# Performance work log

Measured on AMD Instinct MI355X. Metric: run time of the kernel, lower is better.

## Reference

```python
import jax, jax.numpy as jnp
import numpy as np

D, H, N, BS = 3072, 2048, 16, 512
MAX_LATENT_VAR = 0.1


def setup_inputs() -> dict:
    key = jax.random.key(0)
    ks = jax.random.split(key, 12)
    s = 0.02
    return {
        "x": jax.random.normal(ks[0], (BS, D), dtype=jnp.float32),
        "eps": jax.random.normal(ks[1], (1, BS, N), dtype=jnp.float32),
        "enc_W1": jax.random.normal(ks[2], (D, H), dtype=jnp.float32) * s,
        "enc_b1": jnp.zeros((H,), dtype=jnp.float32),
        "enc_Wmu": jax.random.normal(ks[3], (H, N), dtype=jnp.float32) * s,
        "enc_bmu": jnp.zeros((N,), dtype=jnp.float32),
        "enc_Wls": jax.random.normal(ks[4], (H, 1), dtype=jnp.float32) * s,
        "enc_bls": jnp.zeros((1,), dtype=jnp.float32),
        "dec_W1": jax.random.normal(ks[5], (N, H), dtype=jnp.float32) * 0.1,
        "dec_b1": jnp.zeros((H,), dtype=jnp.float32),
        "dec_W2": jax.random.normal(ks[6], (H, D), dtype=jnp.float32) * s,
        "dec_b2": jnp.zeros((D,), dtype=jnp.float32),
    }


def reference(x, eps, enc_W1, enc_b1, enc_Wmu, enc_bmu, enc_Wls, enc_bls,
              dec_W1, dec_b1, dec_W2, dec_b2):
    bs, Dd = x.shape
    n = dec_W1.shape[0]

    def dec(z):  # smooth 2-layer MLP decoder (supports nested autodiff)
        return jnp.tanh(z @ dec_W1 + dec_b1) @ dec_W2 + dec_b2

    # encoder.forward_with_sigma
    h = jnp.tanh(x @ enc_W1 + enc_b1)
    z_star = h @ enc_Wmu + enc_bmu                      # (bs, n)
    sigma = jnp.exp(h @ enc_Wls + enc_bls)[:, 0]        # (bs,)

    # per-sample Jacobian of decoder: (bs, D, n)
    J = jax.vmap(jax.jacfwd(dec))(z_star)

    # per-sample Hessian of f(z) = stop_grad(d) . d,  d = (x - dec(z)) / sigma
    def f_hess(z, xi, sg):
        d = (xi - dec(z)) / sg
        return jnp.dot(jax.lax.stop_gradient(d), d)
    hess = jax.vmap(jax.hessian(f_hess), in_axes=(0, 0, 0))(z_star, x, sigma)  # (bs,n,n)

    eye = jnp.eye(n, dtype=x.dtype)
    Prec = jnp.einsum('bdi,bdj->bij', J, J) / (sigma ** 2)[:, None, None] + eye + hess

    eigvals = jnp.linalg.eigvalsh(Prec)                 # ascending, (bs, n)
    eigmin = eigvals[:, 0]
    delta = 1.0 / MAX_LATENT_VAR - eigmin               # (bs,)
    Prec = Prec + eye * delta[:, None, None]
    eigvals = eigvals + delta[:, None]

    # upper-triangular Cholesky: U^T U = Prec
    U = jnp.swapaxes(jnp.linalg.cholesky(Prec), -1, -2)  # (bs, n, n)

    def solve1(u, e):  # solve U y = e
        return jax.scipy.linalg.solve_triangular(u, e[:, None], lower=False)[:, 0]
    z_off = jax.vmap(jax.vmap(solve1, in_axes=(0, 0)), in_axes=(None, 0))(U, eps)  # (ne,bs,n)
    z_sample = z_star[None] + z_off

    n_eval = eps.shape[0]
    recon = dec(z_sample.reshape(-1, n)).reshape(n_eval, bs, Dd)
    recon_loss = ((recon - x[None]) ** 2).sum(axis=2).mean(axis=0) / (2.0 * sigma ** 2)
    latent_energy = (z_star ** 2).sum(axis=1) / 2.0 + (1.0 / eigvals).sum(axis=1) / 2.0
    logdet_loss = jnp.log(eigvals).sum(axis=1) / 2.0
    sigma_loss = Dd * jnp.log(sigma)
    neg_log_prob = (recon_loss + latent_energy + logdet_loss + sigma_loss) / Dd
    return (neg_log_prob, recon_loss, latent_energy, logdet_loss, sigma)
```

## Files before the change

### kernel.cpp

```cpp
#include <hip/hip_runtime.h>
#include <hip/hip_bf16.h>
#include <math.h>

#define D_ 3072
#define H_ 2048
#define N_ 16
#define BS_ 512

typedef short s16x8 __attribute__((ext_vector_type(8)));
typedef float f32x4v __attribute__((ext_vector_type(4)));
typedef __hip_bfloat16 bf16;

__device__ __forceinline__ void gload_lds16(const void* g, void* l) {
    __builtin_amdgcn_global_load_lds((const __attribute__((address_space(1))) void*)g,
                                     (__attribute__((address_space(3))) void*)l, 16, 0, 0);
}

__device__ __forceinline__ float bf2f(unsigned short u) {
    unsigned v = (unsigned)u << 16; float f; __builtin_memcpy(&f, &v, 4); return f;
}

__global__ __launch_bounds__(256) void mfma_nt_sk(
    const bf16* __restrict__ A, const bf16* __restrict__ Bt,
    float* __restrict__ C, int M, int N, int K, int KC)
{
    __shared__ __align__(16) bf16 As[128 * 32];
    __shared__ __align__(16) bf16 Bs[128 * 32];
    const int tid = threadIdx.x;
    const int w = tid >> 6, l = tid & 63;
    const int wr = w >> 1, wc = w & 1;
    const int m0 = blockIdx.y * 128, n0 = blockIdx.x * 128;
    const int kbeg = blockIdx.z * KC;

    f32x4v acc[4][4];
    #pragma unroll
    for (int a = 0; a < 4; ++a)
        #pragma unroll
        for (int b = 0; b < 4; ++b) acc[a][b] = (f32x4v){0.f, 0.f, 0.f, 0.f};

    const int srow = l >> 2;
    const int scol = (l & 3) * 8;

    for (int k0 = kbeg; k0 < kbeg + KC; k0 += 32) {
        #pragma unroll
        for (int q = 0; q < 2; ++q) {
            int r0 = w * 32 + q * 16;
            gload_lds16(&A[(size_t)(m0 + r0 + srow) * K + k0 + scol], &As[r0 * 32]);
            gload_lds16(&Bt[(size_t)(n0 + r0 + srow) * K + k0 + scol], &Bs[r0 * 32]);
        }
        __syncthreads();
        s16x8 af[4], bfr[4];
        #pragma unroll
        for (int mf = 0; mf < 4; ++mf)
            af[mf] = *(const s16x8*)&As[(wr * 64 + mf * 16 + (l & 15)) * 32 + (l >> 4) * 8];
        #pragma unroll
        for (int nf = 0; nf < 4; ++nf)
            bfr[nf] = *(const s16x8*)&Bs[(wc * 64 + nf * 16 + (l & 15)) * 32 + (l >> 4) * 8];
        #pragma unroll
        for (int mf = 0; mf < 4; ++mf)
            #pragma unroll
            for (int nf = 0; nf < 4; ++nf)
                acc[mf][nf] = __builtin_amdgcn_mfma_f32_16x16x32_bf16(af[mf], bfr[nf], acc[mf][nf], 0, 0, 0);
        __syncthreads();
    }

    #pragma unroll
    for (int mf = 0; mf < 4; ++mf)
        #pragma unroll
        for (int nf = 0; nf < 4; ++nf) {
            int n = n0 + wc * 64 + nf * 16 + (l & 15);
            #pragma unroll
            for (int r = 0; r < 4; ++r) {
                int m = m0 + wr * 64 + mf * 16 + (l >> 4) * 4 + r;
                atomicAdd(&C[(size_t)m * N + n], acc[mf][nf][r]);
            }
        }
}

__global__ __launch_bounds__(256) void ep_ebf(const float* __restrict__ C,
    const float* __restrict__ bias, const float* __restrict__ X,
    bf16* __restrict__ Eout, int MN, int N)
{
    int base = (blockIdx.x * 256 + threadIdx.x) * 8;
    if (base < MN) {
        float4 c0 = *(const float4*)&C[base];
        float4 c1 = *(const float4*)&C[base + 4];
        float4 x0 = *(const float4*)&X[base];
        float4 x1 = *(const float4*)&X[base + 4];
        int n = base % N;
        float4 b0 = *(const float4*)&bias[n];
        float4 b1 = *(const float4*)&bias[n + 4];
        union { s16x8 v; bf16 e[8]; } u;
        u.e[0] = __float2bfloat16(x0.x - (c0.x + b0.x));
        u.e[1] = __float2bfloat16(x0.y - (c0.y + b0.y));
        u.e[2] = __float2bfloat16(x0.z - (c0.z + b0.z));
        u.e[3] = __float2bfloat16(x0.w - (c0.w + b0.w));
        u.e[4] = __float2bfloat16(x1.x - (c1.x + b1.x));
        u.e[5] = __float2bfloat16(x1.y - (c1.y + b1.y));
        u.e[6] = __float2bfloat16(x1.z - (c1.z + b1.z));
        u.e[7] = __float2bfloat16(x1.w - (c1.w + b1.w));
        *(s16x8*)&Eout[base] = u.v;
    }
}

__global__ __launch_bounds__(256) void ep_recon(const float* __restrict__ C,
    const float* __restrict__ bias, const float* __restrict__ X, float* __restrict__ rls)
{
    int m = blockIdx.x;
    float s = 0.f;
    for (int n = threadIdx.x * 4; n < D_; n += 1024) {
        float4 c = *(const float4*)&C[(size_t)m * D_ + n];
        float4 bb = *(const float4*)&bias[n];
        float4 xx = *(const float4*)&X[(size_t)m * D_ + n];
        float v0 = c.x + bb.x - xx.x, v1 = c.y + bb.y - xx.y;
        float v2 = c.z + bb.z - xx.z, v3 = c.w + bb.w - xx.w;
        s += v0 * v0 + v1 * v1 + v2 * v2 + v3 * v3;
    }
    __shared__ float red[4];
    int wid = threadIdx.x >> 6, lane = threadIdx.x & 63;
    #pragma unroll
    for (int off = 32; off; off >>= 1) s += __shfl_xor(s, off);
    if (lane == 0) red[wid] = s;
    __syncthreads();
    if (threadIdx.x == 0) rls[m] = red[0] + red[1] + red[2] + red[3];
}

__global__ __launch_bounds__(256) void jtj_fused(
    const bf16* __restrict__ Vt, const bf16* __restrict__ W2t,
    float* __restrict__ S, int Mb, int b0)
{
    __shared__ union {
        struct { __align__(16) bf16 As[3][128 * 32]; __align__(16) bf16 Bs[3][128 * 32]; } s;
        __align__(16) bf16 J[128 * 136];
    } u;
    const int tid = threadIdx.x;
    const int w = tid >> 6, l = tid & 63;
    const int wr = w >> 1, wc = w & 1;

    int mb, nbk;
    if ((Mb & 7) == 0) {
        int lin = blockIdx.y * 24 + blockIdx.x;
        int xcd = lin & 7, idx = lin >> 3;
        int mchunk = Mb >> 3;
        mb = xcd * mchunk + idx / 24;
        nbk = idx % 24;
    } else { mb = blockIdx.y; nbk = blockIdx.x; }
    const int m0 = mb * 128, n0 = nbk * 128;

    f32x4v acc[4][4];
    #pragma unroll
    for (int a = 0; a < 4; ++a)
        #pragma unroll
        for (int b = 0; b < 4; ++b) acc[a][b] = (f32x4v){0.f, 0.f, 0.f, 0.f};

    const int strow = tid >> 2;
    const int scb = (((tid & 3) ^ ((tid >> 3) & 3)) << 4);

    auto STAGE = [&](int kt, int bi) {
        const char* a0 = (const char*)Vt  + ((size_t)(m0 + strow) * H_ + kt * 32) * 2 + scb;
        const char* b0p = (const char*)W2t + ((size_t)(n0 + strow) * H_ + kt * 32) * 2 + scb;
        char* la = (char*)u.s.As[bi] + w * 1024;
        char* lb = (char*)u.s.Bs[bi] + w * 1024;
        gload_lds16(a0, la);
        gload_lds16(a0 + (size_t)64 * H_ * 2, la + 4096);
        gload_lds16(b0p, lb);
        gload_lds16(b0p + (size_t)64 * H_ * 2, lb + 4096);
    };

    STAGE(0, 0);
    STAGE(1, 1);

    const int rdcb = (((l >> 4) ^ ((l >> 1) & 3)) << 4);

    for (int kt = 0; kt < H_ / 32; ++kt) {
        __builtin_amdgcn_sched_barrier(0);
        if (kt == H_ / 32 - 1) asm volatile("s_waitcnt vmcnt(0)" ::: "memory");
        else                   asm volatile("s_waitcnt vmcnt(4)" ::: "memory");
        __builtin_amdgcn_s_barrier();
        __builtin_amdgcn_sched_barrier(0);
        const int cur = kt % 3;
        const char* Ab = (const char*)u.s.As[cur];
        const char* Bb = (const char*)u.s.Bs[cur];
        s16x8 af[4], bfr[4];
        #pragma unroll
        for (int mf = 0; mf < 4; ++mf)
            af[mf] = *(const s16x8*)(Ab + (wr * 64 + mf * 16 + (l & 15)) * 64 + rdcb);
        #pragma unroll
        for (int nf = 0; nf < 4; ++nf)
            bfr[nf] = *(const s16x8*)(Bb + (wc * 64 + nf * 16 + (l & 15)) * 64 + rdcb);
        if (kt + 2 < H_ / 32) STAGE(kt + 2, (kt + 2) % 3);
        #pragma unroll
        for (int mf = 0; mf < 4; ++mf)
            #pragma unroll
            for (int nf = 0; nf < 4; ++nf)
                acc[mf][nf] = __builtin_amdgcn_mfma_f32_16x16x32_bf16(af[mf], bfr[nf], acc[mf][nf], 0, 0, 0);
    }

    __syncthreads();
    #pragma unroll
    for (int mf = 0; mf < 4; ++mf) {
        int rbase = wr * 64 + mf * 16 + (l >> 4) * 4;
        #pragma unroll
        for (int nf = 0; nf < 4; ++nf) {
            int col = wc * 64 + nf * 16 + (l & 15);
            #pragma unroll
            for (int r = 0; r < 4; ++r)
                u.J[(rbase + r) * 136 + col] = __float2bfloat16(acc[mf][nf][r]);
        }
    }
    __syncthreads();

    #pragma unroll
    for (int t2 = 0; t2 < 2; ++t2) {
        int bl = w * 2 + t2;
        f32x4v sp = (f32x4v){0.f, 0.f, 0.f, 0.f};
        #pragma unroll
        for (int kq = 0; kq < 4; ++kq) {
            s16x8 fr = *(const s16x8*)&u.J[(bl * 16 + (l & 15)) * 136 + kq * 32 + (l >> 4) * 8];
            sp = __builtin_amdgcn_mfma_f32_16x16x32_bf16(fr, fr, sp, 0, 0, 0);
        }
        int bglob = b0 + mb * 8 + bl;
        #pragma unroll
        for (int r = 0; r < 4; ++r)
            atomicAdd(&S[(size_t)bglob * 256 + ((l >> 4) * 4 + r) * 16 + (l & 15)], sp[r]);
    }
}

__global__ __launch_bounds__(256) void hess_mfma(const float* __restrict__ t,
    const float* __restrict__ g, const bf16* __restrict__ W1b, float* __restrict__ S)
{
    const int w = threadIdx.x >> 6, l = threadIdx.x & 63;
    const int b = blockIdx.x * 4 + w;
    const int row = l & 15, kq = (l >> 4) * 8;

    f32x4v sp = (f32x4v){0.f, 0.f, 0.f, 0.f};
    for (int k0 = 0; k0 < H_; k0 += 32) {
        int kk = k0 + kq;
        s16x8 wf = *(const s16x8*)&W1b[(size_t)row * H_ + kk];
        float4 t0 = *(const float4*)&t[(size_t)b * H_ + kk];
        float4 t1 = *(const float4*)&t[(size_t)b * H_ + kk + 4];
        float4 g0 = *(const float4*)&g[(size_t)b * H_ + kk];
        float4 g1 = *(const float4*)&g[(size_t)b * H_ + kk + 4];
        float wv[8];
        wv[0] = 2.f * g0.x * t0.x * (1.f - t0.x * t0.x);
        wv[1] = 2.f * g0.y * t0.y * (1.f - t0.y * t0.y);
        wv[2] = 2.f * g0.z * t0.z * (1.f - t0.z * t0.z);
        wv[3] = 2.f * g0.w * t0.w * (1.f - t0.w * t0.w);
        wv[4] = 2.f * g1.x * t1.x * (1.f - t1.x * t1.x);
        wv[5] = 2.f * g1.y * t1.y * (1.f - t1.y * t1.y);
        wv[6] = 2.f * g1.z * t1.z * (1.f - t1.z * t1.z);
        wv[7] = 2.f * g1.w * t1.w * (1.f - t1.w * t1.w);
        union { s16x8 v; bf16 e[8]; } af;
        #pragma unroll
        for (int e = 0; e < 8; ++e)
            af.e[e] = __float2bfloat16(wv[e] * bf2f((unsigned short)wf[e]));
        sp = __builtin_amdgcn_mfma_f32_16x16x32_bf16(af.v, wf, sp, 0, 0, 0);
    }
    #pragma unroll
    for (int r = 0; r < 4; ++r)
        S[(size_t)b * 256 + ((l >> 4) * 4 + r) * 16 + (l & 15)] += sp[r];
}

__global__ __launch_bounds__(256) void prep_all(
    const float* __restrict__ x, const float* __restrict__ enc_W1,
    const float* __restrict__ dec_W2, const float* __restrict__ dec_W1,
    bf16* __restrict__ x_bf, bf16* __restrict__ eW1t,
    bf16* __restrict__ W2t, bf16* __restrict__ W2b, bf16* __restrict__ W1b)
{
    __shared__ float tile[64][65];
    const int blk = blockIdx.x;
    const int tid = threadIdx.x;
    if (blk < 768) {
        int i = blk * 256 + tid;
        const float4* p = (const float4*)x + (size_t)i * 2;
        float4 a = p[0], b = p[1];
        union { s16x8 v; bf16 e[8]; } u;
        u.e[0] = __float2bfloat16(a.x); u.e[1] = __float2bfloat16(a.y);
        u.e[2] = __float2bfloat16(a.z); u.e[3] = __float2bfloat16(a.w);
        u.e[4] = __float2bfloat16(b.x); u.e[5] = __float2bfloat16(b.y);
        u.e[6] = __float2bfloat16(b.z); u.e[7] = __float2bfloat16(b.w);
        *(s16x8*)&x_bf[(size_t)i * 8] = u.v;
    } else if (blk < 768 + 1536) {
        int bid = blk - 768;
        int r0 = (bid % 48) * 64, c0 = (bid / 48) * 64;
        int tx = tid & 63, ty = tid >> 6;
        #pragma unroll
        for (int k = 0; k < 16; ++k) {
            int rr = ty * 16 + k;
            tile[rr][tx] = enc_W1[(size_t)(r0 + rr) * H_ + c0 + tx];
        }
        __syncthreads();
        #pragma unroll
        for (int k = 0; k < 16; ++k) {
            int cc = ty * 16 + k;
            eW1t[(size_t)(c0 + cc) * D_ + r0 + tx] = __float2bfloat16(tile[tx][cc]);
        }
    } else if (blk < 768 + 3072) {
        int bid = blk - 768 - 1536;
        int r0 = (bid % 32) * 64, c0 = (bid / 32) * 64;
        int tx = tid & 63, ty = tid >> 6;
        #pragma unroll
        for (int k = 0; k < 16; ++k) {
            int rr = ty * 16 + k;
            float v = dec_W2[(size_t)(r0 + rr) * D_ + c0 + tx];
            tile[rr][tx] = v;
            W2b[(size_t)(r0 + rr) * D_ + c0 + tx] = __float2bfloat16(v);
        }
        __syncthreads();
        #pragma unroll
        for (int k = 0; k < 16; ++k) {
            int cc = ty * 16 + k;
            W2t[(size_t)(c0 + cc) * H_ + r0 + tx] = __float2bfloat16(tile[tx][cc]);
        }
    } else {
        int i = (blk - 768 - 3072) * 256 + tid;
        if (i < N_ * H_ / 8) {
            const float4* p = (const float4*)dec_W1 + (size_t)i * 2;
            float4 a = p[0], b = p[1];
            union { s16x8 v; bf16 e[8]; } u;
            u.e[0] = __float2bfloat16(a.x); u.e[1] = __float2bfloat16(a.y);
            u.e[2] = __float2bfloat16(a.z); u.e[3] = __float2bfloat16(a.w);
            u.e[4] = __float2bfloat16(b.x); u.e[5] = __float2bfloat16(b.y);
            u.e[6] = __float2bfloat16(b.z); u.e[7] = __float2bfloat16(b.w);
            *(s16x8*)&W1b[(size_t)i * 8] = u.v;
        }
    }
}

__global__ __launch_bounds__(256) void zsig_t_kernel(const float* __restrict__ Ch,
    const float* __restrict__ enc_b1, const float* __restrict__ Wmu, const float* __restrict__ bmu,
    const float* __restrict__ Wls, const float* __restrict__ bls,
    const float* __restrict__ dW1, const float* __restrict__ db1,
    float* __restrict__ z_star, float* __restrict__ lsig, float* __restrict__ sigma,
    float* __restrict__ t, bf16* __restrict__ tb)
{
    const int b = blockIdx.x, tid = threadIdx.x;
    float acc[17];
    #pragma unroll
    for (int i = 0; i < 17; ++i) acc[i] = 0.f;
    for (int hh = tid; hh < H_; hh += 256) {
        float hv = tanhf(Ch[(size_t)b * H_ + hh] + enc_b1[hh]);
        const float* wr = &Wmu[(size_t)hh * 16];
        #pragma unroll
        for (int i = 0; i < 16; ++i) acc[i] += hv * wr[i];
        acc[16] += hv * Wls[hh];
    }
    __shared__ float red[17][4];
    __shared__ float zs[16];
    const int wid = tid >> 6, lane = tid & 63;
    #pragma unroll
    for (int i = 0; i < 17; ++i) {
        float v = acc[i];
        #pragma unroll
        for (int off = 32; off; off >>= 1) v += __shfl_xor(v, off);
        if (lane == 0) red[i][wid] = v;
    }
    __syncthreads();
    if (tid < 17) {
        float v = red[tid][0] + red[tid][1] + red[tid][2] + red[tid][3];
        if (tid < 16) { float z = v + bmu[tid]; zs[tid] = z; z_star[(size_t)b * 16 + tid] = z; }
        else { float ls = v + bls[0]; lsig[b] = ls; sigma[b] = expf(ls); }
    }
    __syncthreads();
    for (int hh = tid; hh < H_; hh += 256) {
        float a = db1[hh];
        #pragma unroll
        for (int i = 0; i < 16; ++i) a += zs[i] * dW1[(size_t)i * H_ + hh];
        float tv = tanhf(a);
        t[(size_t)b * H_ + hh] = tv;
        tb[(size_t)b * H_ + hh] = __float2bfloat16(tv);
    }
}

__global__ __launch_bounds__(256) void build_t(const float* __restrict__ z,
    const float* __restrict__ W1, const float* __restrict__ b1, bf16* __restrict__ tb)
{
    __shared__ float zs[16];
    int b = blockIdx.x, tid = threadIdx.x;
    if (tid < 16) zs[tid] = z[(size_t)b * 16 + tid];
    __syncthreads();
    for (int hh = tid; hh < H_; hh += 256) {
        float a = b1[hh];
        #pragma unroll
        for (int i = 0; i < 16; ++i) a += zs[i] * W1[(size_t)i * H_ + hh];
        tb[(size_t)b * H_ + hh] = __float2bfloat16(tanhf(a));
    }
}

__global__ __launch_bounds__(256) void build_vt(const float* __restrict__ t,
    const float* __restrict__ W1, bf16* __restrict__ Vt, int b0)
{
    int bl = blockIdx.x, b = b0 + bl, tid = threadIdx.x;
    __shared__ float u[H_];
    for (int hh = tid; hh < H_; hh += 256) {
        float tv = t[(size_t)b * H_ + hh];
        u[hh] = 1.f - tv * tv;
    }
    __syncthreads();
    size_t base = (size_t)bl * 16 * H_;
    int hh = tid * 8;
    for (int i = 0; i < 16; ++i) {
        union { s16x8 v; bf16 e[8]; } pk;
        #pragma unroll
        for (int k = 0; k < 8; ++k)
            pk.e[k] = __float2bfloat16(u[hh + k] * W1[(size_t)i * H_ + hh + k]);
        *(s16x8*)&Vt[base + (size_t)i * H_ + hh] = pk.v;
    }
}

__global__ __launch_bounds__(64) void solve_kernel(const float* __restrict__ S,
    const float* __restrict__ sigma, const float* __restrict__ z_star,
    const float* __restrict__ eps, float* __restrict__ z_sample, float* __restrict__ d_out)
{
    const int lane = threadIdx.x;
    const int q = lane >> 4;
    const int j = lane & 15;
    const int b = blockIdx.x * 4 + q;

    const float sg = sigma[b];
    const float inv_s2 = 1.0f / (sg * sg);

    float a0[16], a[16];
    #pragma unroll
    for (int r = 0; r < 16; ++r) {
        a0[r] = S[(size_t)b * 256 + r * 16 + j] * inv_s2 + ((r == j) ? 1.0f : 0.0f);
        a[r] = a0[r];
    }

    #pragma unroll
    for (int k = 0; k < 14; ++k) {
        float x[16];
        #pragma unroll
        for (int r = 0; r < 16; ++r) x[r] = __shfl(a[k], r, 16);
        float sig2 = 0.f;
        #pragma unroll
        for (int r = 0; r < 16; ++r) if (r > k + 1) sig2 += x[r] * x[r];
        float x0 = x[k + 1];
        float normx = sqrtf(sig2 + x0 * x0);
        float alpha = (x0 >= 0.f) ? -normx : normx;
        float v[16];
        #pragma unroll
        for (int r = 0; r < 16; ++r)
            v[r] = (r <= k) ? 0.f : ((r == k + 1) ? x0 - alpha : x[r]);
        float vtv = 0.f;
        #pragma unroll
        for (int r = 0; r < 16; ++r) vtv += v[r] * v[r];
        float beta = (vtv > 1e-28f) ? 2.0f / vtv : 0.f;
        float sj = 0.f;
        #pragma unroll
        for (int r = 0; r < 16; ++r) sj += a[r] * v[r];
        float av[16];
        #pragma unroll
        for (int r = 0; r < 16; ++r) av[r] = __shfl(sj, r, 16);
        float vtav = 0.f;
        #pragma unroll
        for (int r = 0; r < 16; ++r) vtav += v[r] * av[r];
        float c = 0.5f * beta * vtav;
        float wv[16];
        #pragma unroll
        for (int r = 0; r < 16; ++r) wv[r] = beta * (av[r] - c * v[r]);
        float vj = (j <= k) ? 0.f : ((j == k + 1) ? a[k] - alpha : a[k]);
        float wj = beta * (sj - c * vj);
        #pragma unroll
        for (int r = 0; r < 16; ++r) a[r] -= v[r] * wj + wv[r] * vj;
    }

    float dg[16], eo[15];
    #pragma unroll
    for (int r = 0; r < 16; ++r) dg[r] = __shfl(a[r], r, 16);
    #pragma unroll
    for (int r = 0; r < 15; ++r) eo[r] = __shfl(a[r + 1], r, 16);

    float lo = 1e30f, hi = 1e30f;
    #pragma unroll
    for (int r = 0; r < 16; ++r) {
        float rad = ((r > 0) ? fabsf(eo[r - 1]) : 0.f) + ((r < 15) ? fabsf(eo[r]) : 0.f);
        lo = fminf(lo, dg[r] - rad);
        hi = fminf(hi, dg[r]);
    }
    lo -= 1e-4f; hi += 1e-4f;

    #pragma unroll
    for (int pass = 0; pass < 5; ++pass) {
        float step = (hi - lo) * (1.0f / 17.0f);
        float s = lo + step * (float)(j + 1);
        float qq = dg[0] - s;
        int cnt = (qq < 0.f) ? 1 : 0;
        #pragma unroll
        for (int i = 1; i < 16; ++i) {
            float denom = (fabsf(qq) < 1e-30f) ? -1e-30f : qq;
            qq = dg[i] - s - eo[i - 1] * eo[i - 1] / denom;
            cnt += (qq < 0.f) ? 1 : 0;
        }
        unsigned long long bal = __ballot(cnt >= 1);
        unsigned grp = (unsigned)((bal >> (q * 16)) & 0xffffull);
        int f = grp ? (__ffs(grp) - 1) : 16;
        float nlo = lo + step * (float)f;
        float nhi = (f < 16) ? (lo + step * (float)(f + 1)) : hi;
        lo = nlo; hi = nhi;
    }
    const float lam_min = 0.5f * (lo + hi);
    const float delta = 10.0f - lam_min;

    float bm[16];
    #pragma unroll
    for (int r = 0; r < 16; ++r) bm[r] = a0[r] + ((r == j) ? delta : 0.f);

    float ldsum = 0.f;
    #pragma unroll
    for (int kk = 0; kk < 16; ++kk) {
        float ck[16];
        #pragma unroll
        for (int r = 0; r < 16; ++r) ck[r] = __shfl(bm[kk], r, 16);
        float dkk = sqrtf(fmaxf(ck[kk], 1e-30f));
        float inv = 1.0f / dkk;
        ldsum += logf(dkk);
        float lfull[16];
        #pragma unroll
        for (int r = 0; r < 16; ++r) lfull[r] = ck[r] * inv;
        float lj = bm[kk] * inv;
        if (j == kk) {
            #pragma unroll
            for (int r = 0; r < 16; ++r) bm[r] = (r >= kk) ? lfull[r] : 0.f;
        } else if (j > kk) {
            #pragma unroll
            for (int r = 0; r < 16; ++r)
                if (r > kk) bm[r] -= lfull[r] * lj;
        }
    }

    float w[16];
    #pragma unroll
    for (int r = 0; r < 16; ++r) w[r] = 0.f;
    #pragma unroll
    for (int i = 0; i < 16; ++i) {
        float row[16];
        #pragma unroll
        for (int kx = 0; kx < 16; ++kx) row[kx] = __shfl(bm[i], kx, 16);
        float sacc = 0.f;
        #pragma unroll
        for (int kx = 0; kx < 16; ++kx) if (kx < i) sacc += row[kx] * w[kx];
        float invd = 1.0f / row[i];
        float val = (i == j) ? invd : (-sacc * invd);
        w[i] = (i >= j) ? val : 0.f;
    }

    float tsum = 0.f;
    #pragma unroll
    for (int r = 0; r < 16; ++r) tsum += w[r] * w[r];
    float zv = z_star[(size_t)b * 16 + j];
    float ep = eps[(size_t)b * 16 + j];
    float epsv[16];
    #pragma unroll
    for (int r = 0; r < 16; ++r) epsv[r] = __shfl(ep, r, 16);
    float zoff = 0.f;
    #pragma unroll
    for (int r = 0; r < 16; ++r) zoff += w[r] * epsv[r];
    z_sample[(size_t)b * 16 + j] = zv + zoff;

    float zsq = zv * zv;
    #pragma unroll
    for (int off = 1; off < 16; off <<= 1) {
        tsum += __shfl_xor(tsum, off);
        zsq  += __shfl_xor(zsq, off);
    }
    if (j == 0) {
        d_out[2 * 512 + b] = 0.5f * zsq + 0.5f * tsum;
        d_out[3 * 512 + b] = ldsum;
        d_out[4 * 512 + b] = sg;
    }
}

__global__ void finalize_kernel(const float* __restrict__ rlsum, const float* __restrict__ sigma,
    const float* __restrict__ lsig, float* __restrict__ d_out)
{
    int b = blockIdx.x * 256 + threadIdx.x;
    if (b < BS_) {
        float sg = sigma[b];
        float rl = rlsum[b] / (2.0f * sg * sg);
        float le = d_out[2 * 512 + b];
        float ld = d_out[3 * 512 + b];
        d_out[b] = (rl + le + ld) / 3072.0f + lsig[b];
        d_out[512 + b] = rl;
    }
}

extern "C" void kernel_launch(void* const* d_in, const int* in_sizes, int n_in,
                              void* d_out, int out_size, void* d_ws, size_t ws_size,
                              hipStream_t stream)
{
    const float* x       = (const float*)d_in[0];
    const float* eps     = (const float*)d_in[1];
    const float* enc_W1  = (const float*)d_in[2];
    const float* enc_b1  = (const float*)d_in[3];
    const float* enc_Wmu = (const float*)d_in[4];
    const float* enc_bmu = (const float*)d_in[5];
    const float* enc_Wls = (const float*)d_in[6];
    const float* enc_bls = (const float*)d_in[7];
    const float* dec_W1  = (const float*)d_in[8];
    const float* dec_b1  = (const float*)d_in[9];
    const float* dec_W2  = (const float*)d_in[10];
    const float* dec_b2  = (const float*)d_in[11];
    float* out = (float*)d_out;

    char* wsb = (char*)d_ws;
    size_t off = 0;
    auto alloc = [&](size_t bytes) -> void* {
        off = (off + 255) & ~(size_t)255;
        void* p = wsb + off;
        off += bytes;
        return p;
    };

    float* Ch   = (float*)alloc((size_t)BS_ * H_ * 4);
    float* Cd   = (float*)alloc((size_t)BS_ * D_ * 4);
    float* g    = (float*)alloc((size_t)BS_ * H_ * 4);
    float* S    = (float*)alloc((size_t)BS_ * 256 * 4);
    size_t zero_span = (size_t)((char*)(S + BS_ * 256) - (char*)Ch);

    float* t    = (float*)alloc((size_t)BS_ * H_ * 4);
    float* z_st = (float*)alloc((size_t)BS_ * 16 * 4);
    float* lsig = (float*)alloc(BS_ * 4);
    float* sigm = (float*)alloc(BS_ * 4);
    float* z_sm = (float*)alloc((size_t)BS_ * 16 * 4);
    float* rls  = (float*)alloc(BS_ * 4);
    bf16* x_bf  = (bf16*)alloc((size_t)BS_ * D_ * 2);
    bf16* eW1t  = (bf16*)alloc((size_t)H_ * D_ * 2);
    bf16* W2b   = (bf16*)alloc((size_t)H_ * D_ * 2);
    bf16* W2t   = (bf16*)alloc((size_t)D_ * H_ * 2);
    bf16* W1b   = (bf16*)alloc((size_t)N_ * H_ * 2);
    bf16* t_bf  = (bf16*)alloc((size_t)BS_ * H_ * 2);
    bf16* e_bf  = (bf16*)alloc((size_t)BS_ * D_ * 2);
    bf16* t2b   = (bf16*)alloc((size_t)BS_ * H_ * 2);

    int nb = 0;
    size_t base_off = off;
    const int cand[3] = {512, 128, 32};
    bf16* Vt = nullptr;
    for (int ci = 0; ci < 3; ++ci) {
        off = base_off;
        int n = cand[ci];
        bf16* vt = (bf16*)alloc((size_t)n * 16 * H_ * 2);
        if (off <= ws_size) { nb = n; Vt = vt; break; }
    }
    if (nb == 0) return;

    prep_all<<<dim3(768 + 3072 + 16), 256, 0, stream>>>(
        x, enc_W1, dec_W2, dec_W1, x_bf, eW1t, W2t, W2b, W1b);
    hipMemsetAsync(Ch, 0, zero_span, stream);

    mfma_nt_sk<<<dim3(H_ / 128, BS_ / 128, 4), 256, 0, stream>>>(
        x_bf, eW1t, Ch, BS_, H_, D_, D_ / 4);
    zsig_t_kernel<<<dim3(BS_), 256, 0, stream>>>(Ch, enc_b1, enc_Wmu, enc_bmu, enc_Wls, enc_bls,
        dec_W1, dec_b1, z_st, lsig, sigm, t, t_bf);
    mfma_nt_sk<<<dim3(D_ / 128, BS_ / 128, 4), 256, 0, stream>>>(
        t_bf, W2t, Cd, BS_, D_, H_, H_ / 4);
    ep_ebf<<<dim3(BS_ * D_ / 8 / 256), 256, 0, stream>>>(Cd, dec_b2, x, e_bf, BS_ * D_, D_);
    mfma_nt_sk<<<dim3(H_ / 128, BS_ / 128, 4), 256, 0, stream>>>(
        e_bf, W2b, g, BS_, H_, D_, D_ / 4);

    for (int b0 = 0; b0 < BS_; b0 += nb) {
        build_vt<<<dim3(nb), 256, 0, stream>>>(t, dec_W1, Vt, b0);
        jtj_fused<<<dim3(D_ / 128, nb * 16 / 128), 256, 0, stream>>>(
            Vt, W2t, S, nb * 16 / 128, b0);
    }
    hess_mfma<<<dim3(BS_ / 4), 256, 0, stream>>>(t, g, W1b, S);

    solve_kernel<<<dim3(BS_ / 4), 64, 0, stream>>>(S, sigm, z_st, eps, z_sm, out);
    build_t<<<dim3(BS_), 256, 0, stream>>>(z_sm, dec_W1, dec_b1, t2b);
    hipMemsetAsync(Cd, 0, (size_t)BS_ * D_ * 4, stream);
    mfma_nt_sk<<<dim3(D_ / 128, BS_ / 128, 4), 256, 0, stream>>>(
        t2b, W2t, Cd, BS_, D_, H_, H_ / 4);
    ep_recon<<<dim3(BS_), 256, 0, stream>>>(Cd, dec_b2, x, rls);
    finalize_kernel<<<dim3(2), 256, 0, stream>>>(rls, sigm, lsig, out);
}
```

Before: 359.5 us.

## Replace split-K atomics with per-slice slabs and fuse Vt build and finalize

Three of the four split-K GEMMs now write each K slice to its own fp32 slab with plain stores instead of atomicAdd, and the consumer kernels (zsig_t, ep_ebf, ep_recon) sum the four slabs. This removes the atomic traffic and the large memsets of the Ch and Cd buffers. The Vt construction is fused into zsig_t_kernel when the whole batch fits, which drops the separate build_vt launches, and finalize is folded into ep_recon. In exchange it uses four times the scratch memory for these outputs, and consumers must read four times as much data.

```diff
diff --git a/kernel.cpp b/kernel.cpp
--- a/kernel.cpp
+++ b/kernel.cpp
@@ -20,7 +20,7 @@
     unsigned v = (unsigned)u << 16; float f; __builtin_memcpy(&f, &v, 4); return f;
 }
 
-__global__ __launch_bounds__(256) void mfma_nt_sk(
+__global__ __launch_bounds__(256) void mfma_nt_slab(
     const bf16* __restrict__ A, const bf16* __restrict__ Bt,
     float* __restrict__ C, int M, int N, int K, int KC)
 {
@@ -31,6 +31,7 @@
     const int wr = w >> 1, wc = w & 1;
     const int m0 = blockIdx.y * 128, n0 = blockIdx.x * 128;
     const int kbeg = blockIdx.z * KC;
+    float* Cz = C + (size_t)blockIdx.z * M * N;
 
     f32x4v acc[4][4];
     #pragma unroll
@@ -72,48 +73,120 @@
             #pragma unroll
             for (int r = 0; r < 4; ++r) {
                 int m = m0 + wr * 64 + mf * 16 + (l >> 4) * 4 + r;
+                Cz[(size_t)m * N + n] = acc[mf][nf][r];
+            }
+        }
+}
+
+__global__ __launch_bounds__(256) void mfma_nt_sk(
+    const bf16* __restrict__ A, const bf16* __restrict__ Bt,
+    float* __restrict__ C, int M, int N, int K, int KC)
+{
+    __shared__ __align__(16) bf16 As[128 * 32];
+    __shared__ __align__(16) bf16 Bs[128 * 32];
+    const int tid = threadIdx.x;
+    const int w = tid >> 6, l = tid & 63;
+    const int wr = w >> 1, wc = w & 1;
+    const int m0 = blockIdx.y * 128, n0 = blockIdx.x * 128;
+    const int kbeg = blockIdx.z * KC;
+
+    f32x4v acc[4][4];
+    #pragma unroll
+    for (int a = 0; a < 4; ++a)
+        #pragma unroll
+        for (int b = 0; b < 4; ++b) acc[a][b] = (f32x4v){0.f, 0.f, 0.f, 0.f};
+
+    const int srow = l >> 2;
+    const int scol = (l & 3) * 8;
+
+    for (int k0 = kbeg; k0 < kbeg + KC; k0 += 32) {
+        #pragma unroll
+        for (int q = 0; q < 2; ++q) {
+            int r0 = w * 32 + q * 16;
+            gload_lds16(&A[(size_t)(m0 + r0 + srow) * K + k0 + scol], &As[r0 * 32]);
+            gload_lds16(&Bt[(size_t)(n0 + r0 + srow) * K + k0 + scol], &Bs[r0 * 32]);
+        }
+        __syncthreads();
+        s16x8 af[4], bfr[4];
+        #pragma unroll
+        for (int mf = 0; mf < 4; ++mf)
+            af[mf] = *(const s16x8*)&As[(wr * 64 + mf * 16 + (l & 15)) * 32 + (l >> 4) * 8];
+        #pragma unroll
+        for (int nf = 0; nf < 4; ++nf)
+            bfr[nf] = *(const s16x8*)&Bs[(wc * 64 + nf * 16 + (l & 15)) * 32 + (l >> 4) * 8];
+        #pragma unroll
+        for (int mf = 0; mf < 4; ++mf)
+            #pragma unroll
+            for (int nf = 0; nf < 4; ++nf)
+                acc[mf][nf] = __builtin_amdgcn_mfma_f32_16x16x32_bf16(af[mf], bfr[nf], acc[mf][nf], 0, 0, 0);
+        __syncthreads();
+    }
+
+    #pragma unroll
+    for (int mf = 0; mf < 4; ++mf)
+        #pragma unroll
+        for (int nf = 0; nf < 4; ++nf) {
+            int n = n0 + wc * 64 + nf * 16 + (l & 15);
+            #pragma unroll
+            for (int r = 0; r < 4; ++r) {
+                int m = m0 + wr * 64 + mf * 16 + (l >> 4) * 4 + r;
                 atomicAdd(&C[(size_t)m * N + n], acc[mf][nf][r]);
             }
         }
 }
 
-__global__ __launch_bounds__(256) void ep_ebf(const float* __restrict__ C,
+__global__ __launch_bounds__(256) void ep_ebf(const float* __restrict__ C4,
     const float* __restrict__ bias, const float* __restrict__ X,
     bf16* __restrict__ Eout, int MN, int N)
 {
+    const size_t SL = (size_t)MN;
     int base = (blockIdx.x * 256 + threadIdx.x) * 8;
     if (base < MN) {
-        float4 c0 = *(const float4*)&C[base];
-        float4 c1 = *(const float4*)&C[base + 4];
+        float4 c0 = *(const float4*)&C4[base];
+        float4 c1 = *(const float4*)&C4[base + 4];
+        float4 d0 = *(const float4*)&C4[SL + base];
+        float4 d1 = *(const float4*)&C4[SL + base + 4];
+        float4 e0 = *(const float4*)&C4[2*SL + base];
+        float4 e1 = *(const float4*)&C4[2*SL + base + 4];
+        float4 f0 = *(const float4*)&C4[3*SL + base];
+        float4 f1 = *(const float4*)&C4[3*SL + base + 4];
         float4 x0 = *(const float4*)&X[base];
         float4 x1 = *(const float4*)&X[base + 4];
         int n = base % N;
         float4 b0 = *(const float4*)&bias[n];
         float4 b1 = *(const float4*)&bias[n + 4];
         union { s16x8 v; bf16 e[8]; } u;
-        u.e[0] = __float2bfloat16(x0.x - (c0.x + b0.x));
-        u.e[1] = __float2bfloat16(x0.y - (c0.y + b0.y));
-        u.e[2] = __float2bfloat16(x0.z - (c0.z + b0.z));
-        u.e[3] = __float2bfloat16(x0.w - (c0.w + b0.w));
-        u.e[4] = __float2bfloat16(x1.x - (c1.x + b1.x));
-        u.e[5] = __float2bfloat16(x1.y - (c1.y + b1.y));
-        u.e[6] = __float2bfloat16(x1.z - (c1.z + b1.z));
-        u.e[7] = __float2bfloat16(x1.w - (c1.w + b1.w));
+        u.e[0] = __float2bfloat16(x0.x - (c0.x + d0.x + e0.x + f0.x + b0.x));
+        u.e[1] = __float2bfloat16(x0.y - (c0.y + d0.y + e0.y + f0.y + b0.y));
+        u.e[2] = __float2bfloat16(x0.z - (c0.z + d0.z + e0.z + f0.z + b0.z));
+        u.e[3] = __float2bfloat16(x0.w - (c0.w + d0.w + e0.w + f0.w + b0.w));
+        u.e[4] = __float2bfloat16(x1.x - (c1.x + d1.x + e1.x + f1.x + b1.x));
+        u.e[5] = __float2bfloat16(x1.y - (c1.y + d1.y + e1.y + f1.y + b1.y));
+        u.e[6] = __float2bfloat16(x1.z - (c1.z + d1.z + e1.z + f1.z + b1.z));
+        u.e[7] = __float2bfloat16(x1.w - (c1.w + d1.w + e1.w + f1.w + b1.w));
         *(s16x8*)&Eout[base] = u.v;
     }
 }
 
-__global__ __launch_bounds__(256) void ep_recon(const float* __restrict__ C,
-    const float* __restrict__ bias, const float* __restrict__ X, float* __restrict__ rls)
-{
+__global__ __launch_bounds__(256) void ep_recon_fin(const float* __restrict__ C4,
+    const float* __restrict__ bias, const float* __restrict__ X,
+    const float* __restrict__ sigma, const float* __restrict__ lsig, float* __restrict__ d_out)
+{
+    const size_t SL = (size_t)BS_ * D_;
     int m = blockIdx.x;
     float s = 0.f;
     for (int n = threadIdx.x * 4; n < D_; n += 1024) {
-        float4 c = *(const float4*)&C[(size_t)m * D_ + n];
+        size_t i = (size_t)m * D_ + n;
+        float4 c0 = *(const float4*)&C4[i];
+        float4 c1 = *(const float4*)&C4[SL + i];
+        float4 c2 = *(const float4*)&C4[2*SL + i];
+        float4 c3 = *(const float4*)&C4[3*SL + i];
         float4 bb = *(const float4*)&bias[n];
-        float4 xx = *(const float4*)&X[(size_t)m * D_ + n];
-        float v0 = c.x + bb.x - xx.x, v1 = c.y + bb.y - xx.y;
-        float v2 = c.z + bb.z - xx.z, v3 = c.w + bb.w - xx.w;
+        float4 xx = *(const float4*)&X[i];
+        float v0 = c0.x + c1.x + c2.x + c3.x + bb.x - xx.x;
+        float v1 = c0.y + c1.y + c2.y + c3.y + bb.y - xx.y;
+        float v2 = c0.z + c1.z + c2.z + c3.z + bb.z - xx.z;
+        float v3 = c0.w + c1.w + c2.w + c3.w + bb.w - xx.w;
         s += v0 * v0 + v1 * v1 + v2 * v2 + v3 * v3;
     }
     __shared__ float red[4];
@@ -122,7 +195,15 @@
     for (int off = 32; off; off >>= 1) s += __shfl_xor(s, off);
     if (lane == 0) red[wid] = s;
     __syncthreads();
-    if (threadIdx.x == 0) rls[m] = red[0] + red[1] + red[2] + red[3];
+    if (threadIdx.x == 0) {
+        float tot = red[0] + red[1] + red[2] + red[3];
+        float sg = sigma[m];
+        float rl = tot / (2.0f * sg * sg);
+        float le = d_out[2 * 512 + m];
+        float ld = d_out[3 * 512 + m];
+        d_out[m] = (rl + le + ld) / 3072.0f + lsig[m];
+        d_out[512 + m] = rl;
+    }
 }
 
 __global__ __launch_bounds__(256) void jtj_fused(
@@ -327,19 +408,22 @@
     }
 }
 
-__global__ __launch_bounds__(256) void zsig_t_kernel(const float* __restrict__ Ch,
+__global__ __launch_bounds__(256) void zsig_t_kernel(const float* __restrict__ Ch4,
     const float* __restrict__ enc_b1, const float* __restrict__ Wmu, const float* __restrict__ bmu,
     const float* __restrict__ Wls, const float* __restrict__ bls,
     const float* __restrict__ dW1, const float* __restrict__ db1,
     float* __restrict__ z_star, float* __restrict__ lsig, float* __restrict__ sigma,
-    float* __restrict__ t, bf16* __restrict__ tb)
+    float* __restrict__ t, bf16* __restrict__ tb, bf16* __restrict__ Vt)
 {
     const int b = blockIdx.x, tid = threadIdx.x;
+    const size_t SL = (size_t)BS_ * H_;
     float acc[17];
     #pragma unroll
     for (int i = 0; i < 17; ++i) acc[i] = 0.f;
     for (int hh = tid; hh < H_; hh += 256) {
-        float hv = tanhf(Ch[(size_t)b * H_ + hh] + enc_b1[hh]);
+        size_t idx = (size_t)b * H_ + hh;
+        float c = Ch4[idx] + Ch4[SL + idx] + Ch4[2*SL + idx] + Ch4[3*SL + idx];
+        float hv = tanhf(c + enc_b1[hh]);
         const float* wr = &Wmu[(size_t)hh * 16];
         #pragma unroll
         for (int i = 0; i < 16; ++i) acc[i] += hv * wr[i];
@@ -347,6 +431,7 @@
     }
     __shared__ float red[17][4];
     __shared__ float zs[16];
+    __shared__ float us[H_];
     const int wid = tid >> 6, lane = tid & 63;
     #pragma unroll
     for (int i = 0; i < 17; ++i) {
@@ -369,6 +454,19 @@
         float tv = tanhf(a);
         t[(size_t)b * H_ + hh] = tv;
         tb[(size_t)b * H_ + hh] = __float2bfloat16(tv);
+        us[hh] = 1.f - tv * tv;
+    }
+    if (Vt) {
+        __syncthreads();
+        size_t base = (size_t)b * 16 * H_;
+        int hh = tid * 8;
+        for (int i = 0; i < 16; ++i) {
+            union { s16x8 v; bf16 e[8]; } pk;
+            #pragma unroll
+            for (int k = 0; k < 8; ++k)
+                pk.e[k] = __float2bfloat16(us[hh + k] * dW1[(size_t)i * H_ + hh + k]);
+            *(s16x8*)&Vt[base + (size_t)i * H_ + hh] = pk.v;
+        }
     }
 }
 
@@ -568,20 +666,6 @@
         d_out[2 * 512 + b] = 0.5f * zsq + 0.5f * tsum;
         d_out[3 * 512 + b] = ldsum;
         d_out[4 * 512 + b] = sg;
-    }
-}
-
-__global__ void finalize_kernel(const float* __restrict__ rlsum, const float* __restrict__ sigma,
-    const float* __restrict__ lsig, float* __restrict__ d_out)
-{
-    int b = blockIdx.x * 256 + threadIdx.x;
-    if (b < BS_) {
-        float sg = sigma[b];
-        float rl = rlsum[b] / (2.0f * sg * sg);
-        float le = d_out[2 * 512 + b];
-        float ld = d_out[3 * 512 + b];
-        d_out[b] = (rl + le + ld) / 3072.0f + lsig[b];
-        d_out[512 + b] = rl;
     }
 }
 
@@ -612,18 +696,17 @@
         return p;
     };
 
-    float* Ch   = (float*)alloc((size_t)BS_ * H_ * 4);
-    float* Cd   = (float*)alloc((size_t)BS_ * D_ * 4);
     float* g    = (float*)alloc((size_t)BS_ * H_ * 4);
     float* S    = (float*)alloc((size_t)BS_ * 256 * 4);
-    size_t zero_span = (size_t)((char*)(S + BS_ * 256) - (char*)Ch);
-
+    size_t zero_span = (size_t)((char*)(S + BS_ * 256) - (char*)g);
+
+    float* Ch4  = (float*)alloc((size_t)4 * BS_ * H_ * 4);
+    float* Cd4  = (float*)alloc((size_t)4 * BS_ * D_ * 4);
     float* t    = (float*)alloc((size_t)BS_ * H_ * 4);
     float* z_st = (float*)alloc((size_t)BS_ * 16 * 4);
     float* lsig = (float*)alloc(BS_ * 4);
     float* sigm = (float*)alloc(BS_ * 4);
     float* z_sm = (float*)alloc((size_t)BS_ * 16 * 4);
-    float* rls  = (float*)alloc(BS_ * 4);
     bf16* x_bf  = (bf16*)alloc((size_t)BS_ * D_ * 2);
     bf16* eW1t  = (bf16*)alloc((size_t)H_ * D_ * 2);
     bf16* W2b   = (bf16*)alloc((size_t)H_ * D_ * 2);
@@ -644,33 +727,37 @@
         if (off <= ws_size) { nb = n; Vt = vt; break; }
     }
     if (nb == 0) return;
+    bf16* Vt_full = (nb == 512) ? Vt : nullptr;
 
     prep_all<<<dim3(768 + 3072 + 16), 256, 0, stream>>>(
         x, enc_W1, dec_W2, dec_W1, x_bf, eW1t, W2t, W2b, W1b);
-    hipMemsetAsync(Ch, 0, zero_span, stream);
-
-    mfma_nt_sk<<<dim3(H_ / 128, BS_ / 128, 4), 256, 0, stream>>>(
-        x_bf, eW1t, Ch, BS_, H_, D_, D_ / 4);
-    zsig_t_kernel<<<dim3(BS_), 256, 0, stream>>>(Ch, enc_b1, enc_Wmu, enc_bmu, enc_Wls, enc_bls,
-        dec_W1, dec_b1, z_st, lsig, sigm, t, t_bf);
-    mfma_nt_sk<<<dim3(D_ / 128, BS_ / 128, 4), 256, 0, stream>>>(
-        t_bf, W2t, Cd, BS_, D_, H_, H_ / 4);
-    ep_ebf<<<dim3(BS_ * D_ / 8 / 256), 256, 0, stream>>>(Cd, dec_b2, x, e_bf, BS_ * D_, D_);
+    hipMemsetAsync(g, 0, zero_span, stream);
+
+    mfma_nt_slab<<<dim3(H_ / 128, BS_ / 128, 4), 256, 0, stream>>>(
+        x_bf, eW1t, Ch4, BS_, H_, D_, D_ / 4);
+    zsig_t_kernel<<<dim3(BS_), 256, 0, stream>>>(Ch4, enc_b1, enc_Wmu, enc_bmu, enc_Wls, enc_bls,
+        dec_W1, dec_b1, z_st, lsig, sigm, t, t_bf, Vt_full);
+    mfma_nt_slab<<<dim3(D_ / 128, BS_ / 128, 4), 256, 0, stream>>>(
+        t_bf, W2t, Cd4, BS_, D_, H_, H_ / 4);
+    ep_ebf<<<dim3(BS_ * D_ / 8 / 256), 256, 0, stream>>>(Cd4, dec_b2, x, e_bf, BS_ * D_, D_);
     mfma_nt_sk<<<dim3(H_ / 128, BS_ / 128, 4), 256, 0, stream>>>(
         e_bf, W2b, g, BS_, H_, D_, D_ / 4);
 
-    for (int b0 = 0; b0 < BS_; b0 += nb) {
-        build_vt<<<dim3(nb), 256, 0, stream>>>(t, dec_W1, Vt, b0);
-        jtj_fused<<<dim3(D_ / 128, nb * 16 / 128), 256, 0, stream>>>(
-            Vt, W2t, S, nb * 16 / 128, b0);
+    if (Vt_full) {
+        jtj_fused<<<dim3(D_ / 128, 512 * 16 / 128), 256, 0, stream>>>(
+            Vt_full, W2t, S, 512 * 16 / 128, 0);
+    } else {
+        for (int b0 = 0; b0 < BS_; b0 += nb) {
+            build_vt<<<dim3(nb), 256, 0, stream>>>(t, dec_W1, Vt, b0);
+            jtj_fused<<<dim3(D_ / 128, nb * 16 / 128), 256, 0, stream>>>(
+                Vt, W2t, S, nb * 16 / 128, b0);
+        }
     }
     hess_mfma<<<dim3(BS_ / 4), 256, 0, stream>>>(t, g, W1b, S);
 
     solve_kernel<<<dim3(BS_ / 4), 64, 0, stream>>>(S, sigm, z_st, eps, z_sm, out);
     build_t<<<dim3(BS_), 256, 0, stream>>>(z_sm, dec_W1, dec_b1, t2b);
-    hipMemsetAsync(Cd, 0, (size_t)BS_ * D_ * 4, stream);
-    mfma_nt_sk<<<dim3(D_ / 128, BS_ / 128, 4), 256, 0, stream>>>(
-        t2b, W2t, Cd, BS_, D_, H_, H_ / 4);
-    ep_recon<<<dim3(BS_), 256, 0, stream>>>(Cd, dec_b2, x, rls);
-    finalize_kernel<<<dim3(2), 256, 0, stream>>>(rls, sigm, lsig, out);
-}
+    mfma_nt_slab<<<dim3(D_ / 128, BS_ / 128, 4), 256, 0, stream>>>(
+        t2b, W2t, Cd4, BS_, D_, H_, H_ / 4);
+    ep_recon_fin<<<dim3(BS_), 256, 0, stream>>>(Cd4, dec_b2, x, sigm, lsig, out);
+}
```

Result: faster. 322.1 us (-10.4%).
